# Kernel optimization log

Hardware: AMD Instinct MI355X
Metric: run time of the kernel (lower is better)

## Reference

```python
import jax, jax.numpy as jnp
import numpy as np

EMBED_DIM = 512
NUM_HEADS = 8
HEAD_DIM = EMBED_DIM // NUM_HEADS  # 64


def setup_inputs() -> dict:
    key = jax.random.key(0)
    ks = jax.random.split(key, 9)
    B, N, E, H, D = 4, 1024, EMBED_DIM, NUM_HEADS, HEAD_DIM
    s = 1.0 / np.sqrt(E)  # ~ nn.Linear init scale
    x = jax.random.normal(ks[0], (B, N, E), dtype=jnp.float32)
    # weights stored as (in, out): y = x @ W + b (same math as torch x @ W.T)
    Wq = jax.random.uniform(ks[1], (E, E), jnp.float32, -s, s)
    bq = jax.random.uniform(ks[2], (E,), jnp.float32, -s, s)
    Wk = jax.random.uniform(ks[3], (E, E), jnp.float32, -s, s)
    bk = jax.random.uniform(ks[4], (E,), jnp.float32, -s, s)
    Wv = jax.random.uniform(ks[5], (E, E), jnp.float32, -s, s)
    bv = jax.random.uniform(ks[6], (E,), jnp.float32, -s, s)
    Wg = jax.random.uniform(ks[7], (E, H * D * D), jnp.float32, -s, s)
    bg = jax.random.uniform(ks[8], (H * D * D,), jnp.float32, -s, s)
    return {"x": x, "Wq": Wq, "bq": bq, "Wk": Wk, "bk": bk,
            "Wv": Wv, "bv": bv, "Wg": Wg, "bg": bg}


def reference(x, Wq, bq, Wk, bk, Wv, bv, Wg, bg):
    B, N, E = x.shape
    H, D = NUM_HEADS, HEAD_DIM
    # per-token generated transform g: [B, N, H, D, D] (act = exact GELU)
    g = jax.nn.gelu(x @ Wg + bg, approximate=False).reshape(B, N, H, D, D)
    q = (x @ Wq + bq).reshape(B, N, H, D)
    k = (x @ Wk + bk).reshape(B, N, H, D)
    v = (x @ Wv + bv).reshape(B, N, H, D)
    # q' = q @ g  (per-token, per-head 1xD @ DxD)
    qg = jnp.einsum("bnhd,bnhde->bnhe", q, g)
    # attention scores (note: no 1/sqrt(d) scaling in the original)
    att = jnp.einsum("bnhe,bmhe->bhnm", qg, k)
    att = jax.nn.softmax(att, axis=-1)
    out = jnp.einsum("bhnm,bmhd->bnhd", att, v)
    return out.reshape(B, N, E)
```

## Files before the change

kernel.cpp:

```cpp
#include <hip/hip_runtime.h>
#include <math.h>

#define TOK   4096
#define EDIM  512
#define HEADS 8
#define DHEAD 64
#define GCOLS 32768

typedef unsigned short u16;
typedef _Float16 f16;
typedef __attribute__((ext_vector_type(8))) f16 f16x8;
typedef __attribute__((ext_vector_type(4))) f16 f16x4;
typedef __attribute__((ext_vector_type(4))) float f32x4;
typedef __attribute__((ext_vector_type(4))) unsigned short u16x4;

typedef const __attribute__((address_space(1))) void* gas_ptr;
typedef __attribute__((address_space(3))) void* las_ptr;

__device__ __forceinline__ void gll16(const void* g, void* lds) {
  __builtin_amdgcn_global_load_lds((gas_ptr)g, (las_ptr)lds, 16, 0, 0);
}

#define WAITV(N) asm volatile("s_waitcnt vmcnt(" #N ")" ::: "memory")
__device__ __forceinline__ void barrier_raw() { asm volatile("s_barrier" ::: "memory"); }

__device__ __forceinline__ u16 f2h_bits(float f) {
  union { f16 h; u16 u; } v; v.h = (f16)f;
  return v.u;
}

__device__ __forceinline__ float fast_gelu(float x) {
  float s = x * 0.7071067811865475f;
  float ax = fabsf(s);
  float t = __builtin_amdgcn_rcpf(1.0f + 0.3275911f * ax);
  float poly = t * (0.254829592f + t * (-0.284496736f + t * (1.421413741f +
               t * (-1.453152027f + t * 1.061405429f))));
  float e = __expf(-ax * ax);
  float r = 1.0f - poly * e;
  float erfv = copysignf(r, s);
  return 0.5f * x * (1.0f + erfv);
}

__global__ void cast_f16_k(const float* __restrict__ in, u16* __restrict__ out, int n) {
  int i = (blockIdx.x * blockDim.x + threadIdx.x) * 4;
  if (i + 3 < n) {
    float4 f = *(const float4*)(in + i);
    u16x4 h;
    h.x = f2h_bits(f.x); h.y = f2h_bits(f.y);
    h.z = f2h_bits(f.z); h.w = f2h_bits(f.w);
    *(u16x4*)(out + i) = h;
  }
}

__global__ void transpose_f16_k(const float* __restrict__ in, u16* __restrict__ out,
                                int K, int N) {
  __shared__ float tile[32][33];
  int n0 = blockIdx.x * 32, k0 = blockIdx.y * 32;
  int tx = threadIdx.x, ty = threadIdx.y;
  #pragma unroll
  for (int i = 0; i < 4; i++)
    tile[ty + i * 8][tx] = in[(size_t)(k0 + ty + i * 8) * N + n0 + tx];
  __syncthreads();
  #pragma unroll
  for (int i = 0; i < 4; i++)
    out[(size_t)(n0 + ty + i * 8) * K + k0 + tx] = f2h_bits(tile[tx][ty + i * 8]);
}

__global__ __launch_bounds__(256, 2) void qkv_gemm_k(
    const u16* __restrict__ xf, const u16* __restrict__ Wqt,
    const u16* __restrict__ Wkt, const u16* __restrict__ Wvt,
    const float* __restrict__ bq, const float* __restrict__ bk, const float* __restrict__ bv,
    u16* __restrict__ qho, u16* __restrict__ ko, u16* __restrict__ vTo) {
  __shared__ __align__(16) u16 As[2][16 * 512];
  __shared__ __align__(16) u16 Bs[2][16 * 512];
  const int which = blockIdx.z;
  const u16* Wt = which == 0 ? Wqt : (which == 1 ? Wkt : Wvt);
  const float* bias = which == 0 ? bq : (which == 1 ? bk : bv);
  const int m0 = blockIdx.x * 128;
  const int n0 = blockIdx.y * 128;
  const int tid = threadIdx.x;
  const int w = tid >> 6, lane = tid & 63, l15 = lane & 15, quad = lane >> 4;
  const int mhalf = w >> 1, nhalf = w & 1;

  f32x4 acc[4][4];
  #pragma unroll
  for (int i = 0; i < 4; i++)
    #pragma unroll
    for (int j = 0; j < 4; j++) acc[i][j] = f32x4{0.f, 0.f, 0.f, 0.f};

  auto stage = [&](int d, int kk) {
    #pragma unroll
    for (int i = 0; i < 8; i++) {
      int cb = w * 8 + i;
      if (cb < 16) {
        int ks = cb >> 3, mt = cb & 7;
        gll16(xf + (size_t)(m0 + mt * 16 + l15) * 512 + kk + ks * 32 + quad * 8,
              As[d] + cb * 512);
      } else {
        int bi = cb - 16, ks = bi >> 3, nt = bi & 7;
        gll16(Wt + (size_t)(n0 + nt * 16 + l15) * 512 + kk + ks * 32 + quad * 8,
              Bs[d] + bi * 512);
      }
    }
  };

  stage(0, 0);
  int cur = 0;
  for (int kt = 0; kt < 8; kt++) {
    if (kt < 7) { stage(cur ^ 1, (kt + 1) * 64); WAITV(8); }
    else        { WAITV(0); }
    barrier_raw();
    const u16* Asb = As[cur];
    const u16* Bsb = Bs[cur];
    #pragma unroll
    for (int ks = 0; ks < 2; ks++) {
      f16x8 a[4], b[4];
      #pragma unroll
      for (int mt = 0; mt < 4; mt++)
        a[mt] = *(const f16x8*)(Asb + (ks * 8 + mhalf * 4 + mt) * 512 + lane * 8);
      #pragma unroll
      for (int nt = 0; nt < 4; nt++)
        b[nt] = *(const f16x8*)(Bsb + (ks * 8 + nhalf * 4 + nt) * 512 + lane * 8);
      #pragma unroll
      for (int mt = 0; mt < 4; mt++)
        #pragma unroll
        for (int nt = 0; nt < 4; nt++)
          acc[mt][nt] = __builtin_amdgcn_mfma_f32_16x16x32_f16(a[mt], b[nt], acc[mt][nt], 0, 0, 0);
    }
    barrier_raw();
    cur ^= 1;
  }
  #pragma unroll
  for (int nt = 0; nt < 4; nt++) {
    int col = n0 + (nhalf * 4 + nt) * 16 + l15;
    float bia = bias[col];
    int h = col >> 6, d = col & 63;
    #pragma unroll
    for (int mt = 0; mt < 4; mt++) {
      #pragma unroll
      for (int r = 0; r < 4; r++) {
        int t = m0 + (mhalf * 4 + mt) * 16 + quad * 4 + r;
        int b_ = t >> 10, n = t & 1023;
        float val = acc[mt][nt][r] + bia;
        size_t idx = (((size_t)(b_ * 8 + h) * 1024) + n) * 64 + d;
        if (which == 0)      qho[idx] = f2h_bits(val);
        else if (which == 1) ko[idx] = f2h_bits(val);
        else                 vTo[(((size_t)(b_ * 8 + h) * 64) + d) * 1024 + n] = f2h_bits(val);
      }
    }
  }
}

__global__ __launch_bounds__(256, 2) void qg_fused_k(
    const u16* __restrict__ xf, const u16* __restrict__ Wgt,
    const u16* __restrict__ bgh, const u16* __restrict__ qh,
    float* __restrict__ qgp) {
  __shared__ __align__(16) u16 As[2][16 * 512];
  __shared__ __align__(16) u16 Bs[2][16 * 512];
  __shared__ __align__(16) f16 Qs[128 * 16];
  __shared__ __align__(16) f16 bgs[16 * 64];
  const int bid = blockIdx.x;
  const int dq = bid & 3, head = (bid >> 2) & 7;
  const int t0 = (bid >> 5) * 128;
  const int tid = threadIdx.x;
  const int w = tid >> 6, lane = tid & 63, l15 = lane & 15, quad = lane >> 4;
  const int mhalf = w >> 1, nhalf = w & 1;
  const int b_ = t0 >> 10, nseq0 = t0 & 1023;
  const int bh = b_ * 8 + head;
  const u16* qbase = qh + (((size_t)bh * 1024) + nseq0) * 64;

  #pragma unroll
  for (int i = 0; i < 2; i++) {
    int job = w * 2 + i; if (job >= 6) job -= 6;
    if (job < 4) {
      gll16(qbase + (size_t)(job * 32 + (lane >> 1)) * 64 + dq * 16 + (lane & 1) * 8,
            (f16*)Qs + job * 512);
    } else {
      int j = job - 4;
      gll16(bgh + (size_t)head * 4096 + (dq * 16 + j * 8 + (lane >> 3)) * 64 + (lane & 7) * 8,
            (f16*)bgs + j * 512);
    }
  }

  auto stage = [&](int d, int s) {
    int jp = s >> 3, kk = (s & 7) << 6;
    const u16* bsrc = Wgt + (size_t)(head * 4096 + (dq * 16 + jp * 2) * 64) * 512;
    #pragma unroll
    for (int i = 0; i < 4; i++) {
      int cb = w * 4 + i, ks = cb >> 3, mt = cb & 7;
      gll16(xf + (size_t)(t0 + mt * 16 + l15) * 512 + kk + ks * 32 + quad * 8,
            As[d] + cb * 512);
    }
    #pragma unroll
    for (int i = 0; i < 4; i++) {
      int bi = w * 4 + i, ks = bi >> 3, nt = bi & 7;
      gll16(bsrc + (size_t)(nt * 16 + l15) * 512 + kk + ks * 32 + quad * 8,
            Bs[d] + bi * 512);
    }
  };

  f32x4 acc[4][4], qgacc[4][4];
  #pragma unroll
  for (int i = 0; i < 4; i++)
    #pragma unroll
    for (int j = 0; j < 4; j++) {
      acc[i][j] = f32x4{0.f, 0.f, 0.f, 0.f};
      qgacc[i][j] = f32x4{0.f, 0.f, 0.f, 0.f};
    }

  stage(0, 0);
  for (int s = 0; s < 64; s++) {
    if (s < 63) { stage((s + 1) & 1, s + 1); WAITV(8); }
    else        { WAITV(0); }
    barrier_raw();
    const u16* Asb = As[s & 1];
    const u16* Bsb = Bs[s & 1];
    #pragma unroll
    for (int ks = 0; ks < 2; ks++) {
      f16x8 a[4], b[4];
      #pragma unroll
      for (int mt = 0; mt < 4; mt++)
        a[mt] = *(const f16x8*)(Asb + (ks * 8 + mhalf * 4 + mt) * 512 + lane * 8);
      #pragma unroll
      for (int nt = 0; nt < 4; nt++)
        b[nt] = *(const f16x8*)(Bsb + (ks * 8 + nhalf * 4 + nt) * 512 + lane * 8);
      #pragma unroll
      for (int mt = 0; mt < 4; mt++)
        #pragma unroll
        for (int nt = 0; nt < 4; nt++)
          acc[mt][nt] = __builtin_amdgcn_mfma_f32_16x16x32_f16(a[mt], b[nt], acc[mt][nt], 0, 0, 0);
    }
    if ((s & 7) == 7) {
      int jp = s >> 3;
      int dloc = jp * 2 + nhalf;
      float bgv[4];
      #pragma unroll
      for (int nt = 0; nt < 4; nt++)
        bgv[nt] = (float)bgs[dloc * 64 + nt * 16 + l15];
      #pragma unroll
      for (int mt = 0; mt < 4; mt++) {
        #pragma unroll
        for (int r = 0; r < 4; r++) {
          int row = mhalf * 64 + mt * 16 + quad * 4 + r;
          float qv = (float)Qs[row * 16 + dloc];
          #pragma unroll
          for (int nt = 0; nt < 4; nt++)
            qgacc[mt][nt][r] += qv * fast_gelu(acc[mt][nt][r] + bgv[nt]);
        }
      }
      #pragma unroll
      for (int i = 0; i < 4; i++)
        #pragma unroll
        for (int j = 0; j < 4; j++) acc[i][j] = f32x4{0.f, 0.f, 0.f, 0.f};
    }
    barrier_raw();
  }
  float* red = (float*)As;
  if (nhalf == 1) {
    #pragma unroll
    for (int mt = 0; mt < 4; mt++)
      #pragma unroll
      for (int r = 0; r < 4; r++) {
        int tok = mhalf * 64 + mt * 16 + quad * 4 + r;
        #pragma unroll
        for (int nt = 0; nt < 4; nt++)
          red[tok * 64 + nt * 16 + l15] = qgacc[mt][nt][r];
      }
  }
  barrier_raw();
  if (nhalf == 0) {
    float* outp = qgp + ((size_t)dq * 32 + bh) * 1024 * 64;
    #pragma unroll
    for (int mt = 0; mt < 4; mt++)
      #pragma unroll
      for (int r = 0; r < 4; r++) {
        int tok = mhalf * 64 + mt * 16 + quad * 4 + r;
        int n = nseq0 + tok;
        #pragma unroll
        for (int nt = 0; nt < 4; nt++)
          outp[(size_t)n * 64 + nt * 16 + l15] =
              qgacc[mt][nt][r] + red[tok * 64 + nt * 16 + l15];
      }
  }
}

__global__ __launch_bounds__(256, 2) void attn_k(
    const float* __restrict__ qgp, const u16* __restrict__ kb,
    const u16* __restrict__ vTb, float* __restrict__ out) {
  __shared__ __align__(16) u16 Ks[2][8 * 512];
  __shared__ __align__(16) u16 Vs[2][8 * 512];
  __shared__ __align__(16) f16 Ps[4][16 * 72];
  const int idx = blockIdx.x;
  const int bh = idx & 31;
  const int qt = idx >> 5;
  const int b_ = bh >> 3, h = bh & 7;
  const int tid = threadIdx.x;
  const int w = tid >> 6, lane = tid & 63, l15 = lane & 15, quad = lane >> 4;

  const float* qgB = qgp + (size_t)bh * 1024 * 64;
  const size_t PS = (size_t)32 * 1024 * 64;
  const u16* kB  = kb  + (size_t)bh * 1024 * 64;
  const u16* vB  = vTb + (size_t)bh * 64 * 1024;

  f16x8 aq[2];
  #pragma unroll
  for (int ks = 0; ks < 2; ks++) {
    size_t off = (size_t)(qt * 64 + w * 16 + l15) * 64 + ks * 32 + quad * 8;
    f16x8 v;
    #pragma unroll
    for (int e = 0; e < 8; e++)
      v[e] = (f16)(qgB[off + e] + qgB[PS + off + e] +
                   qgB[2 * PS + off + e] + qgB[3 * PS + off + e]);
    aq[ks] = v;
  }

  f32x4 o[4];
  #pragma unroll
  for (int i = 0; i < 4; i++) o[i] = f32x4{0.f, 0.f, 0.f, 0.f};
  float m_old[4], l_old[4];
  #pragma unroll
  for (int r = 0; r < 4; r++) { m_old[r] = -1e30f; l_old[r] = 0.f; }

  auto stageKV = [&](int d, int kt) {
    #pragma unroll
    for (int i = 0; i < 2; i++) {
      int cb = w * 2 + i;
      int ks = cb >> 2, nt = cb & 3;
      gll16(kB + (size_t)(kt * 64 + nt * 16 + l15) * 64 + ks * 32 + quad * 8, Ks[d] + cb * 512);
      gll16(vB + (size_t)(nt * 16 + l15) * 1024 + kt * 64 + ks * 32 + quad * 8, Vs[d] + cb * 512);
    }
  };

  stageKV(0, 0);
  int cur = 0;
  for (int kt = 0; kt < 16; kt++) {
    if (kt < 15) { stageKV(cur ^ 1, kt + 1); WAITV(4); }
    else         { WAITV(0); }
    barrier_raw();
    f32x4 s[4];
    #pragma unroll
    for (int nt = 0; nt < 4; nt++) s[nt] = f32x4{0.f, 0.f, 0.f, 0.f};
    #pragma unroll
    for (int ks = 0; ks < 2; ks++)
      #pragma unroll
      for (int nt = 0; nt < 4; nt++) {
        f16x8 kf = *(const f16x8*)(Ks[cur] + (ks * 4 + nt) * 512 + lane * 8);
        s[nt] = __builtin_amdgcn_mfma_f32_16x16x32_f16(aq[ks], kf, s[nt], 0, 0, 0);
      }
    float rmax[4];
    #pragma unroll
    for (int r = 0; r < 4; r++)
      rmax[r] = fmaxf(fmaxf(s[0][r], s[1][r]), fmaxf(s[2][r], s[3][r]));
    #pragma unroll
    for (int off = 1; off < 16; off <<= 1)
      #pragma unroll
      for (int r = 0; r < 4; r++)
        rmax[r] = fmaxf(rmax[r], __shfl_xor(rmax[r], off));
    float alpha[4], rsum[4];
    #pragma unroll
    for (int r = 0; r < 4; r++) {
      float mn = fmaxf(m_old[r], rmax[r]);
      alpha[r] = __expf(m_old[r] - mn);
      m_old[r] = mn;
      rsum[r] = 0.f;
    }
    #pragma unroll
    for (int nt = 0; nt < 4; nt++)
      #pragma unroll
      for (int r = 0; r < 4; r++) {
        float p = __expf(s[nt][r] - m_old[r]);
        rsum[r] += p;
        Ps[w][(quad * 4 + r) * 72 + nt * 16 + l15] = (f16)p;
      }
    #pragma unroll
    for (int off = 1; off < 16; off <<= 1)
      #pragma unroll
      for (int r = 0; r < 4; r++)
        rsum[r] += __shfl_xor(rsum[r], off);
    #pragma unroll
    for (int r = 0; r < 4; r++) l_old[r] = l_old[r] * alpha[r] + rsum[r];
    #pragma unroll
    for (int nt = 0; nt < 4; nt++)
      #pragma unroll
      for (int r = 0; r < 4; r++) o[nt][r] *= alpha[r];
    #pragma unroll
    for (int ks = 0; ks < 2; ks++) {
      f16x8 pa = *(const f16x8*)(&Ps[w][l15 * 72 + ks * 32 + quad * 8]);
      #pragma unroll
      for (int nt = 0; nt < 4; nt++) {
        f16x8 vf = *(const f16x8*)(Vs[cur] + (ks * 4 + nt) * 512 + lane * 8);
        o[nt] = __builtin_amdgcn_mfma_f32_16x16x32_f16(pa, vf, o[nt], 0, 0, 0);
      }
    }
    barrier_raw();
    cur ^= 1;
  }
  #pragma unroll
  for (int r = 0; r < 4; r++) {
    float inv = 1.f / l_old[r];
    int n = qt * 64 + w * 16 + quad * 4 + r;
    #pragma unroll
    for (int nt = 0; nt < 4; nt++)
      out[((size_t)(b_ * 1024 + n)) * 512 + h * 64 + nt * 16 + l15] = o[nt][r] * inv;
  }
}

extern "C" void kernel_launch(void* const* d_in, const int* in_sizes, int n_in,
                              void* d_out, int out_size, void* d_ws, size_t ws_size,
                              hipStream_t stream) {
  const float* x  = (const float*)d_in[0];
  const float* Wq = (const float*)d_in[1];
  const float* bq = (const float*)d_in[2];
  const float* Wk = (const float*)d_in[3];
  const float* bk = (const float*)d_in[4];
  const float* Wv = (const float*)d_in[5];
  const float* bv = (const float*)d_in[6];
  const float* Wg = (const float*)d_in[7];
  const float* bg = (const float*)d_in[8];
  float* out = (float*)d_out;

  const size_t NX = (size_t)TOK * EDIM;
  const size_t NWG = (size_t)GCOLS * EDIM;
  const size_t NW = (size_t)EDIM * EDIM;

  char* p = (char*)d_ws;
  u16* xf  = (u16*)p; p += NX * 2;
  u16* Wgt = (u16*)p; p += NWG * 2;
  u16* Wqt = (u16*)p; p += NW * 2;
  u16* Wkt = (u16*)p; p += NW * 2;
  u16* Wvt = (u16*)p; p += NW * 2;
  u16* qh  = (u16*)p; p += NX * 2;
  u16* kf  = (u16*)p; p += NX * 2;
  u16* vT  = (u16*)p; p += NX * 2;
  float* qgp = (float*)p; p += NX * 4 * 4;
  u16* bgh = (u16*)p; p += GCOLS * 2;

  hipLaunchKernelGGL(cast_f16_k, dim3(NX / 1024), dim3(256), 0, stream,
                     x, xf, (int)NX);
  hipLaunchKernelGGL(cast_f16_k, dim3(GCOLS / 1024), dim3(256), 0, stream,
                     bg, bgh, GCOLS);
  hipLaunchKernelGGL(transpose_f16_k, dim3(EDIM / 32, EDIM / 32), dim3(32, 8), 0, stream,
                     Wq, Wqt, EDIM, EDIM);
  hipLaunchKernelGGL(transpose_f16_k, dim3(EDIM / 32, EDIM / 32), dim3(32, 8), 0, stream,
                     Wk, Wkt, EDIM, EDIM);
  hipLaunchKernelGGL(transpose_f16_k, dim3(EDIM / 32, EDIM / 32), dim3(32, 8), 0, stream,
                     Wv, Wvt, EDIM, EDIM);
  hipLaunchKernelGGL(transpose_f16_k, dim3(GCOLS / 32, EDIM / 32), dim3(32, 8), 0, stream,
                     Wg, Wgt, EDIM, GCOLS);
  hipLaunchKernelGGL(qkv_gemm_k, dim3(TOK / 128, EDIM / 128, 3), dim3(256), 0, stream,
                     xf, Wqt, Wkt, Wvt, bq, bk, bv, qh, kf, vT);
  hipLaunchKernelGGL(qg_fused_k, dim3(1024), dim3(256), 0, stream,
                     xf, Wgt, bgh, qh, qgp);
  hipLaunchKernelGGL(attn_k, dim3(512), dim3(256), 0, stream,
                     qgp, kf, vT, out);
}
```

Before: 464.6 us.

## Single-buffer qg_fused_k LDS staging to raise occupancy to four blocks per CU

Replaces the double-buffered A/B LDS tiles with a single buffer and raises launch bounds from 2 to 4 blocks per CU, so more blocks can hide global-load latency through occupancy rather than software prefetch. The loop now issues the stage load and waits with __syncthreads each iteration, losing load/compute overlap within a block. The higher launch bound also caps registers per thread, which may cause spills given the 32 f32x4 accumulators. Startup loads of Q and bias are reassigned so no job is duplicated.

```diff
diff --git a/kernel.cpp b/kernel.cpp
--- a/kernel.cpp
+++ b/kernel.cpp
@@ -151,14 +151,15 @@
   }
 }
 
-__global__ __launch_bounds__(256, 2) void qg_fused_k(
+__global__ __launch_bounds__(256, 4) void qg_fused_k(
     const u16* __restrict__ xf, const u16* __restrict__ Wgt,
     const u16* __restrict__ bgh, const u16* __restrict__ qh,
     float* __restrict__ qgp) {
-  __shared__ __align__(16) u16 As[2][16 * 512];
-  __shared__ __align__(16) u16 Bs[2][16 * 512];
+  __shared__ __align__(16) u16 ABs[32 * 512];
   __shared__ __align__(16) f16 Qs[128 * 16];
   __shared__ __align__(16) f16 bgs[16 * 64];
+  u16* As = ABs;
+  u16* Bs = ABs + 16 * 512;
   const int bid = blockIdx.x;
   const int dq = bid & 3, head = (bid >> 2) & 7;
   const int t0 = (bid >> 5) * 128;
@@ -171,31 +172,31 @@
 
   #pragma unroll
   for (int i = 0; i < 2; i++) {
-    int job = w * 2 + i; if (job >= 6) job -= 6;
+    int job = w * 2 + i;
     if (job < 4) {
       gll16(qbase + (size_t)(job * 32 + (lane >> 1)) * 64 + dq * 16 + (lane & 1) * 8,
             (f16*)Qs + job * 512);
-    } else {
+    } else if (job < 6) {
       int j = job - 4;
       gll16(bgh + (size_t)head * 4096 + (dq * 16 + j * 8 + (lane >> 3)) * 64 + (lane & 7) * 8,
             (f16*)bgs + j * 512);
     }
   }
 
-  auto stage = [&](int d, int s) {
+  auto stage = [&](int s) {
     int jp = s >> 3, kk = (s & 7) << 6;
     const u16* bsrc = Wgt + (size_t)(head * 4096 + (dq * 16 + jp * 2) * 64) * 512;
     #pragma unroll
     for (int i = 0; i < 4; i++) {
       int cb = w * 4 + i, ks = cb >> 3, mt = cb & 7;
       gll16(xf + (size_t)(t0 + mt * 16 + l15) * 512 + kk + ks * 32 + quad * 8,
-            As[d] + cb * 512);
+            As + cb * 512);
     }
     #pragma unroll
     for (int i = 0; i < 4; i++) {
       int bi = w * 4 + i, ks = bi >> 3, nt = bi & 7;
       gll16(bsrc + (size_t)(nt * 16 + l15) * 512 + kk + ks * 32 + quad * 8,
-            Bs[d] + bi * 512);
+            Bs + bi * 512);
     }
   };
 
@@ -208,22 +209,18 @@
       qgacc[i][j] = f32x4{0.f, 0.f, 0.f, 0.f};
     }
 
-  stage(0, 0);
   for (int s = 0; s < 64; s++) {
-    if (s < 63) { stage((s + 1) & 1, s + 1); WAITV(8); }
-    else        { WAITV(0); }
-    barrier_raw();
-    const u16* Asb = As[s & 1];
-    const u16* Bsb = Bs[s & 1];
+    stage(s);
+    __syncthreads();
     #pragma unroll
     for (int ks = 0; ks < 2; ks++) {
       f16x8 a[4], b[4];
       #pragma unroll
       for (int mt = 0; mt < 4; mt++)
-        a[mt] = *(const f16x8*)(Asb + (ks * 8 + mhalf * 4 + mt) * 512 + lane * 8);
+        a[mt] = *(const f16x8*)(As + (ks * 8 + mhalf * 4 + mt) * 512 + lane * 8);
       #pragma unroll
       for (int nt = 0; nt < 4; nt++)
-        b[nt] = *(const f16x8*)(Bsb + (ks * 8 + nhalf * 4 + nt) * 512 + lane * 8);
+        b[nt] = *(const f16x8*)(Bs + (ks * 8 + nhalf * 4 + nt) * 512 + lane * 8);
       #pragma unroll
       for (int mt = 0; mt < 4; mt++)
         #pragma unroll
@@ -253,9 +250,9 @@
         #pragma unroll
         for (int j = 0; j < 4; j++) acc[i][j] = f32x4{0.f, 0.f, 0.f, 0.f};
     }
-    barrier_raw();
-  }
-  float* red = (float*)As;
+    __syncthreads();
+  }
+  float* red = (float*)ABs;
   if (nhalf == 1) {
     #pragma unroll
     for (int mt = 0; mt < 4; mt++)
@@ -267,7 +264,7 @@
           red[tok * 64 + nt * 16 + l15] = qgacc[mt][nt][r];
       }
   }
-  barrier_raw();
+  __syncthreads();
   if (nhalf == 0) {
     float* outp = qgp + ((size_t)dq * 32 + bh) * 1024 * 64;
     #pragma unroll
```

Measured after the change: 615.9 us. 32.6% more time.
